# Performance work log

Measured on AMD Instinct MI355X. Metric: run time of the kernel, lower is better.

The kernel has to match this reference:

```python
import jax, jax.numpy as jnp
import numpy as np

B, S, D_MODEL, H, D_KV = 2, 2048, 1024, 16, 64
NUM_BUCKETS, MAX_DIST = 32, 128


def _relative_position_bucket(rel_pos, num_buckets=NUM_BUCKETS, max_distance=MAX_DIST):
    # bidirectional (encoder) bucketing, matching T5Attention._relative_position_bucket
    nb = num_buckets // 2
    buckets = (rel_pos > 0).astype(jnp.int32) * nb
    rel = jnp.abs(rel_pos)
    max_exact = nb // 2
    is_small = rel < max_exact
    rel_f = jnp.maximum(rel.astype(jnp.float32), 1.0)  # guard log(0); masked by is_small anyway
    large = max_exact + (
        jnp.log(rel_f / max_exact) / np.log(max_distance / max_exact) * (nb - max_exact)
    ).astype(jnp.int32)
    large = jnp.minimum(large, nb - 1)
    return buckets + jnp.where(is_small, rel, large)


def setup_inputs() -> dict:
    key = jax.random.key(0)
    ks = jax.random.split(key, 6)
    sc = 1.0 / np.sqrt(D_MODEL)
    return {
        "hidden_states": jax.random.normal(ks[0], (B, S, D_MODEL), jnp.float32),
        "Wq": jax.random.normal(ks[1], (D_MODEL, H * D_KV), jnp.float32) * sc,
        "Wk": jax.random.normal(ks[2], (D_MODEL, H * D_KV), jnp.float32) * sc,
        "Wv": jax.random.normal(ks[3], (D_MODEL, H * D_KV), jnp.float32) * sc,
        "Wo": jax.random.normal(ks[4], (H * D_KV, D_MODEL), jnp.float32) * sc,
        "rel_bias_table": jax.random.normal(ks[5], (NUM_BUCKETS, H), jnp.float32),
    }


def reference(hidden_states, Wq, Wk, Wv, Wo, rel_bias_table):
    b, s, _ = hidden_states.shape
    # projections (T5 uses no bias, scale=1.0 in attention)
    q = (hidden_states @ Wq).reshape(b, s, H, D_KV).transpose(0, 2, 1, 3)  # bhsd
    k = (hidden_states @ Wk).reshape(b, s, H, D_KV).transpose(0, 2, 1, 3)
    v = (hidden_states @ Wv).reshape(b, s, H, D_KV).transpose(0, 2, 1, 3)

    # relative position bias: [1, H, S, S]
    ctx = jnp.arange(s)[:, None]
    mem = jnp.arange(s)[None, :]
    buckets = _relative_position_bucket(mem - ctx)          # [S, S]
    pos_bias = rel_bias_table[buckets]                       # [S, S, H]
    pos_bias = pos_bias.transpose(2, 0, 1)[None]             # [1, H, S, S]

    scores = jnp.einsum("bhqd,bhkd->bhqk", q, k) + pos_bias  # scale = 1.0
    probs = jax.nn.softmax(scores, axis=-1)
    attn = jnp.einsum("bhqk,bhkd->bhqd", probs, v)
    attn = attn.transpose(0, 2, 1, 3).reshape(b, s, H * D_KV)
    return attn @ Wo
```

## Files before the change

kernel.cpp:

```cpp
#include <hip/hip_runtime.h>
#include <hip/hip_fp16.h>

#define S_LEN 2048
#define NH 16
#define DK 64
#define DM 1024
#define NB 2
#define QKV_SZ (NB * NH * S_LEN * DK)

typedef _Float16 half8 __attribute__((ext_vector_type(8)));
typedef _Float16 half4v __attribute__((ext_vector_type(4)));
typedef __fp16 fp16x2 __attribute__((ext_vector_type(2)));
typedef float f32x4 __attribute__((ext_vector_type(4)));

static __device__ __forceinline__ half4v pack4(const f32x4 v) {
  fp16x2 lo = __builtin_amdgcn_cvt_pkrtz(v[0], v[1]);
  fp16x2 hi = __builtin_amdgcn_cvt_pkrtz(v[2], v[3]);
  half4v r;
  ((fp16x2*)&r)[0] = lo;
  ((fp16x2*)&r)[1] = hi;
  return r;
}

#define GLL(gp, lp)                                                              \
  __builtin_amdgcn_global_load_lds(                                              \
      (const __attribute__((address_space(1))) unsigned int*)(gp),               \
      (__attribute__((address_space(3))) unsigned int*)(lp), 16, 0, 0)


__global__ __launch_bounds__(256) void conv_f32_f16(const float* __restrict__ in,
                                                    _Float16* __restrict__ out, int n4) {
  int i = blockIdx.x * 256 + threadIdx.x;
  if (i >= n4) return;
  float4 v = ((const float4*)in)[i];
  half4v o;
  o[0] = (_Float16)v.x; o[1] = (_Float16)v.y; o[2] = (_Float16)v.z; o[3] = (_Float16)v.w;
  ((half4v*)out)[i] = o;
}

__global__ __launch_bounds__(256) void transpose_conv4(
    const float* __restrict__ Wq, const float* __restrict__ Wk,
    const float* __restrict__ Wv, const float* __restrict__ Wo,
    _Float16* __restrict__ Wqkvt, _Float16* __restrict__ Wot) {
  __shared__ float tile[32][33];
  int z = blockIdx.z;
  const float* W = (z == 0) ? Wq : (z == 1) ? Wk : (z == 2) ? Wv : Wo;
  _Float16* Wt = (z < 3) ? (Wqkvt + (size_t)z * 1048576) : Wot;
  float scale = (z == 0) ? 1.44269504f : 1.0f;
  int tx = threadIdx.x, ty = threadIdx.y;
  int nx = blockIdx.x * 32 + tx;
  int ky = blockIdx.y * 32;
#pragma unroll
  for (int i = 0; i < 32; i += 8) tile[ty + i][tx] = W[(size_t)(ky + ty + i) * DM + nx];
  __syncthreads();
  int kx = ky + tx;
  int ny = blockIdx.x * 32;
#pragma unroll
  for (int i = 0; i < 32; i += 8)
    Wt[(size_t)(ny + ty + i) * DM + kx] = (_Float16)(tile[tx][ty + i] * scale);
}

__global__ __launch_bounds__(256) void bias_tab_kernel(const float* __restrict__ table,
                                                       float* __restrict__ tab) {
  int i = blockIdx.x * 256 + threadIdx.x;
  if (i >= NH * 4095) return;
  int h = i / 4095, r = i - h * 4095;
  int rel = r - 2047;
  int bucket = rel > 0 ? 16 : 0;
  int a = rel < 0 ? -rel : rel;
  if (a < 8) {
    bucket += a;
  } else {
    int lg = 31 - __clz(a * a);
    int large = 8 + (lg - 6);
    bucket += (large < 15 ? large : 15);
  }
  tab[i] = table[bucket * NH + h] * 1.44269504f;
}

template <int MODE>
__global__ __launch_bounds__(256) void gemm_f16(const _Float16* __restrict__ A,
                                                const _Float16* __restrict__ Bt,
                                                void* __restrict__ Cout,
                                                int M, int N, int K) {
  __shared__ _Float16 As[128 * 32];
  __shared__ _Float16 Bs[128 * 32];
  const int t = threadIdx.x;
  const int m0 = blockIdx.y * 128, n0 = blockIdx.x * 128;
  const int w = t >> 6, lane = t & 63, l15 = lane & 15, quad = lane >> 4;
  const int wr = (w >> 1) * 64, wc = (w & 1) * 64;
  const int swz = (quad ^ (l15 & 3)) * 8;

  f32x4 acc[4][4];
#pragma unroll
  for (int i = 0; i < 4; i++)
#pragma unroll
    for (int j = 0; j < 4; j++) acc[i][j] = (f32x4){0.f, 0.f, 0.f, 0.f};

  for (int k0 = 0; k0 < K; k0 += 32) {
    __syncthreads();
#pragma unroll
    for (int i = 0; i < 2; i++) {
      int id = t + 256 * i;
      int row = id >> 2, c = id & 3;
      int cg = c ^ (row & 3);
      GLL(A + (size_t)(m0 + row) * K + k0 + cg * 8, (char*)As + id * 16);
      GLL(Bt + (size_t)(n0 + row) * K + k0 + cg * 8, (char*)Bs + id * 16);
    }
    __syncthreads();
    half8 af[4], bf[4];
#pragma unroll
    for (int i = 0; i < 4; i++) af[i] = *(const half8*)(As + (wr + i * 16 + l15) * 32 + swz);
#pragma unroll
    for (int i = 0; i < 4; i++) bf[i] = *(const half8*)(Bs + (wc + i * 16 + l15) * 32 + swz);
#pragma unroll
    for (int i = 0; i < 4; i++)
#pragma unroll
      for (int j = 0; j < 4; j++)
        acc[i][j] = __builtin_amdgcn_mfma_f32_16x16x32_f16(af[i], bf[j], acc[i][j], 0, 0, 0);
  }

#pragma unroll
  for (int i = 0; i < 4; i++)
#pragma unroll
    for (int j = 0; j < 4; j++) {
      int row0 = m0 + wr + i * 16 + quad * 4;
      int col = n0 + wc + j * 16 + l15;
      if (MODE == 1) {
#pragma unroll
        for (int r = 0; r < 4; r++)
          ((float*)Cout)[(size_t)(row0 + r) * N + col] = acc[i][j][r];
      } else {
        int which = col >> 10, rem = col & 1023, hh = rem >> 6, dd = rem & 63;
        int bb = row0 >> 11, ss = row0 & 2047;
        _Float16* base = (_Float16*)Cout;
        if (which == 2) {
          *(half4v*)(base + (size_t)2 * QKV_SZ +
                     ((size_t)((bb * NH + hh) * DK + dd)) * S_LEN + ss) = pack4(acc[i][j]);
        } else {
#pragma unroll
          for (int r = 0; r < 4; r++)
            base[(size_t)which * QKV_SZ +
                 ((size_t)((bb * NH + hh) * S_LEN) + ss + r) * DK + dd] = (_Float16)acc[i][j][r];
        }
      }
    }
}

__global__ __launch_bounds__(256, 4) void attn_kernel(
    const _Float16* __restrict__ Q, const _Float16* __restrict__ K,
    const _Float16* __restrict__ Vt, const float* __restrict__ btab,
    _Float16* __restrict__ attn_out) {
  __shared__ _Float16 Ks[4096];
  __shared__ _Float16 Vs[4096];
  __shared__ _Float16 Ps[4][1024];
  __shared__ float slab[512];

  const int t = threadIdx.x;
  const int Q0 = blockIdx.x * 64;
  const int h = blockIdx.y, b = blockIdx.z;
  const int w = t >> 6, lane = t & 63, l15 = lane & 15, quad = lane >> 4;
  const int qw0 = Q0 + w * 16;
  const int sw7 = l15 & 7;

  const _Float16* Qb = Q + (size_t)(b * NH + h) * S_LEN * DK;
  const _Float16* Kb = K + (size_t)(b * NH + h) * S_LEN * DK;
  const _Float16* Vb = Vt + (size_t)(b * NH + h) * S_LEN * DK;

  for (int i = t; i < 512; i += 256) slab[i] = btab[h * 4095 + 1791 + i];

  half8 qf[2];
#pragma unroll
  for (int dh = 0; dh < 2; dh++)
    qf[dh] = *(const half8*)(Qb + (size_t)(qw0 + l15) * DK + dh * 32 + quad * 8);

  f32x4 o[4];
#pragma unroll
  for (int dt = 0; dt < 4; dt++) o[dt] = (f32x4){0.f, 0.f, 0.f, 0.f};
  float m_ = -INFINITY, l_ = 0.f;

  for (int k0 = 0; k0 < S_LEN; k0 += 64) {
#pragma unroll
    for (int i = 0; i < 2; i++) {
      int id = t + 256 * i;
      int row = id >> 3, c = id & 7;
      int cg = c ^ (row & 7);
      GLL(Kb + (size_t)(k0 + row) * DK + cg * 8, (char*)Ks + id * 16);
      GLL(Vb + (size_t)row * S_LEN + k0 + cg * 8, (char*)Vs + id * 16);
    }
    __syncthreads();

    const int dk0 = k0 - qw0;
    const bool farneg = (dk0 <= -191);
    const bool farpos = (dk0 >= 143);
    const bool nearc = !(farneg || farpos);
    const float cb = farneg ? slab[128] : slab[384];

    f32x4 st[4];
    if (nearc) {
#pragma unroll
      for (int kt = 0; kt < 4; kt++) {
        int i0 = dk0 + kt * 16 + quad * 4 - l15 + 256;
        f32x4 v;
        v[0] = slab[i0]; v[1] = slab[i0 + 1]; v[2] = slab[i0 + 2]; v[3] = slab[i0 + 3];
        st[kt] = v;
      }
    } else {
#pragma unroll
      for (int kt = 0; kt < 4; kt++) st[kt] = (f32x4){0.f, 0.f, 0.f, 0.f};
    }

    half8 kf[4][2], vf[4][2];
#pragma unroll
    for (int kt = 0; kt < 4; kt++)
#pragma unroll
      for (int dh = 0; dh < 2; dh++)
        kf[kt][dh] = *(const half8*)(&Ks[(kt * 16 + l15) * 64 + (((dh << 2) + quad) ^ sw7) * 8]);
#pragma unroll
    for (int dt = 0; dt < 4; dt++)
#pragma unroll
      for (int kh = 0; kh < 2; kh++)
        vf[dt][kh] = *(const half8*)(&Vs[(dt * 16 + l15) * 64 + (((kh << 2) + quad) ^ sw7) * 8]);

#pragma unroll
    for (int kt = 0; kt < 4; kt++)
#pragma unroll
      for (int dh = 0; dh < 2; dh++)
        st[kt] = __builtin_amdgcn_mfma_f32_16x16x32_f16(kf[kt][dh], qf[dh], st[kt], 0, 0, 0);

    float cm = fmaxf(fmaxf(st[0][0], st[0][1]), fmaxf(st[0][2], st[0][3]));
#pragma unroll
    for (int kt = 1; kt < 4; kt++)
      cm = fmaxf(cm, fmaxf(fmaxf(st[kt][0], st[kt][1]), fmaxf(st[kt][2], st[kt][3])));
    cm = fmaxf(cm, __shfl_xor(cm, 16));
    cm = fmaxf(cm, __shfl_xor(cm, 32));
    float mc = nearc ? cm : cm + cb;
    if (__any(mc > m_)) {
      float mnew = fmaxf(m_, mc);
      float alpha = __builtin_amdgcn_exp2f(m_ - mnew);
      m_ = mnew;
      l_ *= alpha;
#pragma unroll
      for (int dt = 0; dt < 4; dt++) o[dt] *= alpha;
    }
    float msub = nearc ? m_ : m_ - cb;

    f32x4 lacc = (f32x4){0.f, 0.f, 0.f, 0.f};
#pragma unroll
    for (int kt = 0; kt < 4; kt++) {
      f32x4 p;
#pragma unroll
      for (int r = 0; r < 4; r++) p[r] = __builtin_amdgcn_exp2f(st[kt][r] - msub);
      lacc += p;
      int g = 2 * kt + (quad >> 1);
      *(half4v*)(&Ps[w][l15 * 64 + (g ^ sw7) * 8 + (quad & 1) * 4]) = pack4(p);
    }
    l_ += (lacc[0] + lacc[1]) + (lacc[2] + lacc[3]);
    __asm__ volatile("s_waitcnt lgkmcnt(0)" ::: "memory");

    half8 pf[2];
#pragma unroll
    for (int kh = 0; kh < 2; kh++)
      pf[kh] = *(const half8*)(&Ps[w][l15 * 64 + (((kh << 2) + quad) ^ sw7) * 8]);
#pragma unroll
    for (int dt = 0; dt < 4; dt++)
#pragma unroll
      for (int kh = 0; kh < 2; kh++)
        o[dt] = __builtin_amdgcn_mfma_f32_16x16x32_f16(vf[dt][kh], pf[kh], o[dt], 0, 0, 0);
    __syncthreads();
  }

  float lf = l_;
  lf += __shfl_xor(lf, 16);
  lf += __shfl_xor(lf, 32);
  float inv = 1.0f / lf;
  int q = qw0 + l15;
#pragma unroll
  for (int dt = 0; dt < 4; dt++) {
    f32x4 ov = o[dt] * inv;
    *(half4v*)(attn_out + ((size_t)(b * S_LEN + q)) * DM + h * DK + dt * 16 + quad * 4) =
        pack4(ov);
  }
}

extern "C" void kernel_launch(void* const* d_in, const int* in_sizes, int n_in,
                              void* d_out, int out_size, void* d_ws, size_t ws_size,
                              hipStream_t stream) {
  const float* hs  = (const float*)d_in[0];
  const float* Wq  = (const float*)d_in[1];
  const float* Wk  = (const float*)d_in[2];
  const float* Wv  = (const float*)d_in[3];
  const float* Wo  = (const float*)d_in[4];
  const float* tbl = (const float*)d_in[5];
  float* out = (float*)d_out;
  char* ws = (char*)d_ws;

  _Float16* Xh    = (_Float16*)(ws);
  _Float16* Wqkvt = (_Float16*)(ws + (8u << 20));
  _Float16* Wot   = (_Float16*)(ws + (14u << 20));
  _Float16* Qd    = (_Float16*)(ws + (16u << 20));
  _Float16* Kd    = Qd + (size_t)QKV_SZ;
  _Float16* Vd    = Qd + (size_t)2 * QKV_SZ;
  _Float16* Ah    = (_Float16*)(ws + (40u << 20));
  float*    btab  = (float*)(ws + (48u << 20));

  conv_f32_f16<<<4096, 256, 0, stream>>>(hs, Xh, (NB * S_LEN * DM) / 4);
  transpose_conv4<<<dim3(32, 32, 4), dim3(32, 8), 0, stream>>>(Wq, Wk, Wv, Wo, Wqkvt, Wot);
  bias_tab_kernel<<<256, 256, 0, stream>>>(tbl, btab);

  gemm_f16<0><<<dim3(24, 32), 256, 0, stream>>>(Xh, Wqkvt, (void*)Qd, NB * S_LEN, 3 * DM, DM);
  attn_kernel<<<dim3(S_LEN / 64, NH, NB), 256, 0, stream>>>(Qd, Kd, Vd, btab, Ah);
  gemm_f16<1><<<dim3(8, 32), 256, 0, stream>>>(Ah, Wot, (void*)out, NB * S_LEN, DM, DM);
}
```

Measured before the change: 216.8 us.

## Split attention keys across waves, swap GEMM MFMA operands, merge prep kernels

The attention kernel now has each wave cover all 64 queries of the block but only a quarter of every 128-key chunk. K and V fragments are read straight from global memory instead of staged through LDS, which removes the per-iteration barriers. The per-wave softmax partials are merged at the end through a shared-memory max/sum reduction. The QKV/output GEMMs swap MFMA operands so Q/K and fp32 outputs are written as contiguous vectors, and the bias-table kernel is folded into the weight transpose launch. The trade-off is more registers (occupancy hint lowered to 3), uncoalesced-ish direct global loads, and extra end-of-kernel reduction work.

```diff
diff --git a/kernel.cpp b/kernel.cpp
--- a/kernel.cpp
+++ b/kernel.cpp
@@ -38,16 +38,36 @@
   ((half4v*)out)[i] = o;
 }
 
-__global__ __launch_bounds__(256) void transpose_conv4(
+__global__ __launch_bounds__(256) void prep_kernel(
     const float* __restrict__ Wq, const float* __restrict__ Wk,
     const float* __restrict__ Wv, const float* __restrict__ Wo,
-    _Float16* __restrict__ Wqkvt, _Float16* __restrict__ Wot) {
+    _Float16* __restrict__ Wqkvt, _Float16* __restrict__ Wot,
+    const float* __restrict__ table, float* __restrict__ btab) {
+  int z = blockIdx.z;
+  int tx = threadIdx.x, ty = threadIdx.y;
+  if (z == 4) {
+    int bid = blockIdx.y * 32 + blockIdx.x;
+    if (bid >= 256) return;
+    int i = bid * 256 + ty * 32 + tx;
+    if (i >= NH * 4095) return;
+    int h = i / 4095, r = i - h * 4095;
+    int rel = r - 2047;
+    int bucket = rel > 0 ? 16 : 0;
+    int a = rel < 0 ? -rel : rel;
+    if (a < 8) {
+      bucket += a;
+    } else {
+      int lg = 31 - __clz(a * a);
+      int large = 8 + (lg - 6);
+      bucket += (large < 15 ? large : 15);
+    }
+    btab[i] = table[bucket * NH + h] * 1.44269504f;
+    return;
+  }
   __shared__ float tile[32][33];
-  int z = blockIdx.z;
   const float* W = (z == 0) ? Wq : (z == 1) ? Wk : (z == 2) ? Wv : Wo;
   _Float16* Wt = (z < 3) ? (Wqkvt + (size_t)z * 1048576) : Wot;
   float scale = (z == 0) ? 1.44269504f : 1.0f;
-  int tx = threadIdx.x, ty = threadIdx.y;
   int nx = blockIdx.x * 32 + tx;
   int ky = blockIdx.y * 32;
 #pragma unroll
@@ -58,24 +78,6 @@
 #pragma unroll
   for (int i = 0; i < 32; i += 8)
     Wt[(size_t)(ny + ty + i) * DM + kx] = (_Float16)(tile[tx][ty + i] * scale);
-}
-
-__global__ __launch_bounds__(256) void bias_tab_kernel(const float* __restrict__ table,
-                                                       float* __restrict__ tab) {
-  int i = blockIdx.x * 256 + threadIdx.x;
-  if (i >= NH * 4095) return;
-  int h = i / 4095, r = i - h * 4095;
-  int rel = r - 2047;
-  int bucket = rel > 0 ? 16 : 0;
-  int a = rel < 0 ? -rel : rel;
-  if (a < 8) {
-    bucket += a;
-  } else {
-    int lg = 31 - __clz(a * a);
-    int large = 8 + (lg - 6);
-    bucket += (large < 15 ? large : 15);
-  }
-  tab[i] = table[bucket * NH + h] * 1.44269504f;
 }
 
 template <int MODE>
@@ -90,6 +92,7 @@
   const int w = t >> 6, lane = t & 63, l15 = lane & 15, quad = lane >> 4;
   const int wr = (w >> 1) * 64, wc = (w & 1) * 64;
   const int swz = (quad ^ (l15 & 3)) * 8;
+  const bool swapped = (MODE == 1) || (n0 < 2048);
 
   f32x4 acc[4][4];
 #pragma unroll
@@ -113,55 +116,64 @@
     for (int i = 0; i < 4; i++) af[i] = *(const half8*)(As + (wr + i * 16 + l15) * 32 + swz);
 #pragma unroll
     for (int i = 0; i < 4; i++) bf[i] = *(const half8*)(Bs + (wc + i * 16 + l15) * 32 + swz);
-#pragma unroll
-    for (int i = 0; i < 4; i++)
-#pragma unroll
-      for (int j = 0; j < 4; j++)
-        acc[i][j] = __builtin_amdgcn_mfma_f32_16x16x32_f16(af[i], bf[j], acc[i][j], 0, 0, 0);
+    if (swapped) {
+#pragma unroll
+      for (int i = 0; i < 4; i++)
+#pragma unroll
+        for (int j = 0; j < 4; j++)
+          acc[i][j] = __builtin_amdgcn_mfma_f32_16x16x32_f16(bf[j], af[i], acc[i][j], 0, 0, 0);
+    } else {
+#pragma unroll
+      for (int i = 0; i < 4; i++)
+#pragma unroll
+        for (int j = 0; j < 4; j++)
+          acc[i][j] = __builtin_amdgcn_mfma_f32_16x16x32_f16(af[i], bf[j], acc[i][j], 0, 0, 0);
+    }
   }
 
 #pragma unroll
   for (int i = 0; i < 4; i++)
 #pragma unroll
     for (int j = 0; j < 4; j++) {
-      int row0 = m0 + wr + i * 16 + quad * 4;
-      int col = n0 + wc + j * 16 + l15;
       if (MODE == 1) {
-#pragma unroll
-        for (int r = 0; r < 4; r++)
-          ((float*)Cout)[(size_t)(row0 + r) * N + col] = acc[i][j][r];
+        int srow = m0 + wr + i * 16 + l15;
+        int col0 = n0 + wc + j * 16 + quad * 4;
+        *(f32x4*)((float*)Cout + (size_t)srow * N + col0) = acc[i][j];
+      } else if (n0 < 2048) {
+        int srow = m0 + wr + i * 16 + l15;
+        int col0 = n0 + wc + j * 16 + quad * 4;
+        int which = col0 >> 10, rem = col0 & 1023, hh = rem >> 6, dd = rem & 63;
+        int bb = srow >> 11, ss = srow & 2047;
+        _Float16* base = (_Float16*)Cout;
+        *(half4v*)(base + (size_t)which * QKV_SZ +
+                   ((size_t)((bb * NH + hh) * S_LEN) + ss) * DK + dd) = pack4(acc[i][j]);
       } else {
-        int which = col >> 10, rem = col & 1023, hh = rem >> 6, dd = rem & 63;
+        int row0 = m0 + wr + i * 16 + quad * 4;
+        int col = n0 + wc + j * 16 + l15;
+        int rem = col & 1023, hh = rem >> 6, dd = rem & 63;
         int bb = row0 >> 11, ss = row0 & 2047;
         _Float16* base = (_Float16*)Cout;
-        if (which == 2) {
-          *(half4v*)(base + (size_t)2 * QKV_SZ +
-                     ((size_t)((bb * NH + hh) * DK + dd)) * S_LEN + ss) = pack4(acc[i][j]);
-        } else {
-#pragma unroll
-          for (int r = 0; r < 4; r++)
-            base[(size_t)which * QKV_SZ +
-                 ((size_t)((bb * NH + hh) * S_LEN) + ss + r) * DK + dd] = (_Float16)acc[i][j][r];
-        }
-      }
-    }
-}
-
-__global__ __launch_bounds__(256, 4) void attn_kernel(
+        *(half4v*)(base + (size_t)2 * QKV_SZ +
+                   ((size_t)((bb * NH + hh) * DK + dd)) * S_LEN + ss) = pack4(acc[i][j]);
+      }
+    }
+}
+
+__global__ __launch_bounds__(256, 3) void attn_kernel(
     const _Float16* __restrict__ Q, const _Float16* __restrict__ K,
     const _Float16* __restrict__ Vt, const float* __restrict__ btab,
     _Float16* __restrict__ attn_out) {
-  __shared__ _Float16 Ks[4096];
-  __shared__ _Float16 Vs[4096];
-  __shared__ _Float16 Ps[4][1024];
-  __shared__ float slab[512];
+  __shared__ __align__(16) char smem[35840];
+  _Float16* Ps = (_Float16*)smem;
+  float* slab = (float*)(smem + 16384);
+  float* obuf = (float*)smem;
+  float* mlbuf = (float*)(smem + 32768);
 
   const int t = threadIdx.x;
   const int Q0 = blockIdx.x * 64;
   const int h = blockIdx.y, b = blockIdx.z;
   const int w = t >> 6, lane = t & 63, l15 = lane & 15, quad = lane >> 4;
-  const int qw0 = Q0 + w * 16;
-  const int sw7 = l15 & 7;
+  const int sw3 = l15 & 3;
 
   const _Float16* Qb = Q + (size_t)(b * NH + h) * S_LEN * DK;
   const _Float16* Kb = K + (size_t)(b * NH + h) * S_LEN * DK;
@@ -169,118 +181,176 @@
 
   for (int i = t; i < 512; i += 256) slab[i] = btab[h * 4095 + 1791 + i];
 
-  half8 qf[2];
-#pragma unroll
-  for (int dh = 0; dh < 2; dh++)
-    qf[dh] = *(const half8*)(Qb + (size_t)(qw0 + l15) * DK + dh * 32 + quad * 8);
-
-  f32x4 o[4];
-#pragma unroll
-  for (int dt = 0; dt < 4; dt++) o[dt] = (f32x4){0.f, 0.f, 0.f, 0.f};
-  float m_ = -INFINITY, l_ = 0.f;
-
-  for (int k0 = 0; k0 < S_LEN; k0 += 64) {
-#pragma unroll
-    for (int i = 0; i < 2; i++) {
-      int id = t + 256 * i;
-      int row = id >> 3, c = id & 7;
-      int cg = c ^ (row & 7);
-      GLL(Kb + (size_t)(k0 + row) * DK + cg * 8, (char*)Ks + id * 16);
-      GLL(Vb + (size_t)row * S_LEN + k0 + cg * 8, (char*)Vs + id * 16);
-    }
-    __syncthreads();
-
-    const int dk0 = k0 - qw0;
-    const bool farneg = (dk0 <= -191);
-    const bool farpos = (dk0 >= 143);
+  half8 qf[4][2];
+#pragma unroll
+  for (int qt = 0; qt < 4; qt++)
+#pragma unroll
+    for (int dh = 0; dh < 2; dh++)
+      qf[qt][dh] =
+          *(const half8*)(Qb + (size_t)(Q0 + qt * 16 + l15) * DK + dh * 32 + quad * 8);
+
+  f32x4 o[4][4];
+#pragma unroll
+  for (int dt = 0; dt < 4; dt++)
+#pragma unroll
+    for (int qt = 0; qt < 4; qt++) o[dt][qt] = (f32x4){0.f, 0.f, 0.f, 0.f};
+  float m_[4] = {-INFINITY, -INFINITY, -INFINITY, -INFINITY};
+  float l_[4] = {0.f, 0.f, 0.f, 0.f};
+
+  _Float16* Pw = Ps + w * 2048;
+
+  __syncthreads();
+
+  for (int it = 0; it < 16; it++) {
+    const int ks0 = it * 128 + w * 32;
+    const int dk = ks0 - Q0;
+    const bool farneg = (dk <= -159);
+    const bool farpos = (dk >= 191);
     const bool nearc = !(farneg || farpos);
     const float cb = farneg ? slab[128] : slab[384];
 
-    f32x4 st[4];
-    if (nearc) {
-#pragma unroll
-      for (int kt = 0; kt < 4; kt++) {
-        int i0 = dk0 + kt * 16 + quad * 4 - l15 + 256;
-        f32x4 v;
-        v[0] = slab[i0]; v[1] = slab[i0 + 1]; v[2] = slab[i0 + 2]; v[3] = slab[i0 + 3];
-        st[kt] = v;
-      }
-    } else {
-#pragma unroll
-      for (int kt = 0; kt < 4; kt++) st[kt] = (f32x4){0.f, 0.f, 0.f, 0.f};
-    }
-
-    half8 kf[4][2], vf[4][2];
-#pragma unroll
-    for (int kt = 0; kt < 4; kt++)
+    half8 kf[2][2], vf[4];
+#pragma unroll
+    for (int kt = 0; kt < 2; kt++)
 #pragma unroll
       for (int dh = 0; dh < 2; dh++)
-        kf[kt][dh] = *(const half8*)(&Ks[(kt * 16 + l15) * 64 + (((dh << 2) + quad) ^ sw7) * 8]);
-#pragma unroll
-    for (int dt = 0; dt < 4; dt++)
-#pragma unroll
-      for (int kh = 0; kh < 2; kh++)
-        vf[dt][kh] = *(const half8*)(&Vs[(dt * 16 + l15) * 64 + (((kh << 2) + quad) ^ sw7) * 8]);
-
-#pragma unroll
-    for (int kt = 0; kt < 4; kt++)
-#pragma unroll
-      for (int dh = 0; dh < 2; dh++)
-        st[kt] = __builtin_amdgcn_mfma_f32_16x16x32_f16(kf[kt][dh], qf[dh], st[kt], 0, 0, 0);
-
-    float cm = fmaxf(fmaxf(st[0][0], st[0][1]), fmaxf(st[0][2], st[0][3]));
-#pragma unroll
-    for (int kt = 1; kt < 4; kt++)
-      cm = fmaxf(cm, fmaxf(fmaxf(st[kt][0], st[kt][1]), fmaxf(st[kt][2], st[kt][3])));
-    cm = fmaxf(cm, __shfl_xor(cm, 16));
-    cm = fmaxf(cm, __shfl_xor(cm, 32));
-    float mc = nearc ? cm : cm + cb;
-    if (__any(mc > m_)) {
-      float mnew = fmaxf(m_, mc);
-      float alpha = __builtin_amdgcn_exp2f(m_ - mnew);
-      m_ = mnew;
-      l_ *= alpha;
-#pragma unroll
-      for (int dt = 0; dt < 4; dt++) o[dt] *= alpha;
-    }
-    float msub = nearc ? m_ : m_ - cb;
-
-    f32x4 lacc = (f32x4){0.f, 0.f, 0.f, 0.f};
-#pragma unroll
-    for (int kt = 0; kt < 4; kt++) {
-      f32x4 p;
-#pragma unroll
-      for (int r = 0; r < 4; r++) p[r] = __builtin_amdgcn_exp2f(st[kt][r] - msub);
-      lacc += p;
-      int g = 2 * kt + (quad >> 1);
-      *(half4v*)(&Ps[w][l15 * 64 + (g ^ sw7) * 8 + (quad & 1) * 4]) = pack4(p);
-    }
-    l_ += (lacc[0] + lacc[1]) + (lacc[2] + lacc[3]);
+        kf[kt][dh] =
+            *(const half8*)(Kb + (size_t)(ks0 + kt * 16 + l15) * DK + dh * 32 + quad * 8);
+#pragma unroll
+    for (int dt = 0; dt < 4; dt++)
+      vf[dt] = *(const half8*)(Vb + (size_t)(dt * 16 + l15) * S_LEN + ks0 + quad * 8);
+
+#pragma unroll
+    for (int qt = 0; qt < 4; qt++) {
+      f32x4 st[2];
+      if (nearc) {
+#pragma unroll
+        for (int kt = 0; kt < 2; kt++) {
+          int i0 = dk + kt * 16 + quad * 4 - qt * 16 - l15 + 256;
+          f32x4 v;
+          v[0] = slab[i0]; v[1] = slab[i0 + 1]; v[2] = slab[i0 + 2]; v[3] = slab[i0 + 3];
+          st[kt] = v;
+        }
+      } else {
+        st[0] = (f32x4){0.f, 0.f, 0.f, 0.f};
+        st[1] = (f32x4){0.f, 0.f, 0.f, 0.f};
+      }
+#pragma unroll
+      for (int kt = 0; kt < 2; kt++)
+#pragma unroll
+        for (int dh = 0; dh < 2; dh++)
+          st[kt] = __builtin_amdgcn_mfma_f32_16x16x32_f16(kf[kt][dh], qf[qt][dh], st[kt],
+                                                          0, 0, 0);
+
+      float cm = fmaxf(fmaxf(st[0][0], st[0][1]), fmaxf(st[0][2], st[0][3]));
+      cm = fmaxf(cm, fmaxf(fmaxf(st[1][0], st[1][1]), fmaxf(st[1][2], st[1][3])));
+      cm = fmaxf(cm, __shfl_xor(cm, 16));
+      cm = fmaxf(cm, __shfl_xor(cm, 32));
+      float mc = nearc ? cm : cm + cb;
+      if (__any(mc > m_[qt])) {
+        float mnew = fmaxf(m_[qt], mc);
+        float alpha = __builtin_amdgcn_exp2f(m_[qt] - mnew);
+        m_[qt] = mnew;
+        l_[qt] *= alpha;
+#pragma unroll
+        for (int dt = 0; dt < 4; dt++) o[dt][qt] *= alpha;
+      }
+      float msub = nearc ? m_[qt] : m_[qt] - cb;
+#pragma unroll
+      for (int kt = 0; kt < 2; kt++) {
+        f32x4 p;
+#pragma unroll
+        for (int r = 0; r < 4; r++) p[r] = __builtin_amdgcn_exp2f(st[kt][r] - msub);
+        l_[qt] += (p[0] + p[1]) + (p[2] + p[3]);
+        int g = kt * 2 + (quad >> 1);
+        *(half4v*)(&Pw[(qt * 16 + l15) * 32 + ((g ^ sw3) << 3) + ((quad & 1) << 2)]) =
+            pack4(p);
+      }
+    }
     __asm__ volatile("s_waitcnt lgkmcnt(0)" ::: "memory");
 
-    half8 pf[2];
-#pragma unroll
-    for (int kh = 0; kh < 2; kh++)
-      pf[kh] = *(const half8*)(&Ps[w][l15 * 64 + (((kh << 2) + quad) ^ sw7) * 8]);
-#pragma unroll
-    for (int dt = 0; dt < 4; dt++)
-#pragma unroll
-      for (int kh = 0; kh < 2; kh++)
-        o[dt] = __builtin_amdgcn_mfma_f32_16x16x32_f16(vf[dt][kh], pf[kh], o[dt], 0, 0, 0);
-    __syncthreads();
-  }
-
-  float lf = l_;
-  lf += __shfl_xor(lf, 16);
-  lf += __shfl_xor(lf, 32);
-  float inv = 1.0f / lf;
-  int q = qw0 + l15;
-#pragma unroll
-  for (int dt = 0; dt < 4; dt++) {
-    f32x4 ov = o[dt] * inv;
-    *(half4v*)(attn_out + ((size_t)(b * S_LEN + q)) * DM + h * DK + dt * 16 + quad * 4) =
-        pack4(ov);
-  }
+    half8 pf[4];
+#pragma unroll
+    for (int qt = 0; qt < 4; qt++)
+      pf[qt] = *(const half8*)(&Pw[(qt * 16 + l15) * 32 + ((quad ^ sw3) << 3)]);
+#pragma unroll
+    for (int dt = 0; dt < 4; dt++)
+#pragma unroll
+      for (int qt = 0; qt < 4; qt++)
+        o[dt][qt] = __builtin_amdgcn_mfma_f32_16x16x32_f16(vf[dt], pf[qt], o[dt][qt],
+                                                           0, 0, 0);
+  }
+
+#pragma unroll
+  for (int qt = 0; qt < 4; qt++) {
+    l_[qt] += __shfl_xor(l_[qt], 16);
+    l_[qt] += __shfl_xor(l_[qt], 32);
+  }
+  __syncthreads();
+  if (quad == 0) {
+#pragma unroll
+    for (int qt = 0; qt < 4; qt++) {
+      mlbuf[(w * 2 + 0) * 64 + qt * 16 + l15] = m_[qt];
+      mlbuf[(w * 2 + 1) * 64 + qt * 16 + l15] = l_[qt];
+    }
+  }
+  __syncthreads();
+  float aw[4], invL[4];
+#pragma unroll
+  for (int qt = 0; qt < 4; qt++) {
+    int q = qt * 16 + l15;
+    float M = mlbuf[0 * 64 + q];
+#pragma unroll
+    for (int v = 1; v < 4; v++) M = fmaxf(M, mlbuf[(v * 2) * 64 + q]);
+    float L = 0.f;
+#pragma unroll
+    for (int v = 0; v < 4; v++)
+      L += mlbuf[(v * 2 + 1) * 64 + q] * __builtin_amdgcn_exp2f(mlbuf[(v * 2) * 64 + q] - M);
+    aw[qt] = __builtin_amdgcn_exp2f(m_[qt] - M);
+    invL[qt] = 1.0f / L;
+  }
+#pragma unroll
+  for (int dt = 0; dt < 4; dt++)
+#pragma unroll
+    for (int qt = 0; qt < 4; qt++) o[dt][qt] *= aw[qt];
+
+#define OIDX(dt, qt) (((qt) * 16 + l15) * 64 + ((((dt) * 4 + quad) ^ ((qt * 16 + l15) & 15)) << 2))
+  if (w & 1) {
+    float* ob = obuf + (w >> 1) * 4096;
+#pragma unroll
+    for (int dt = 0; dt < 4; dt++)
+#pragma unroll
+      for (int qt = 0; qt < 4; qt++) *(f32x4*)(&ob[OIDX(dt, qt)]) = o[dt][qt];
+  }
+  __syncthreads();
+  if (!(w & 1)) {
+    float* ob = obuf + (w >> 1) * 4096;
+#pragma unroll
+    for (int dt = 0; dt < 4; dt++)
+#pragma unroll
+      for (int qt = 0; qt < 4; qt++) o[dt][qt] += *(f32x4*)(&ob[OIDX(dt, qt)]);
+  }
+  __syncthreads();
+  if (w == 2) {
+#pragma unroll
+    for (int dt = 0; dt < 4; dt++)
+#pragma unroll
+      for (int qt = 0; qt < 4; qt++) *(f32x4*)(&obuf[OIDX(dt, qt)]) = o[dt][qt];
+  }
+  __syncthreads();
+  if (w == 0) {
+#pragma unroll
+    for (int qt = 0; qt < 4; qt++) {
+      int q = Q0 + qt * 16 + l15;
+#pragma unroll
+      for (int dt = 0; dt < 4; dt++) {
+        f32x4 ov = (o[dt][qt] + *(f32x4*)(&obuf[OIDX(dt, qt)])) * invL[qt];
+        *(half4v*)(attn_out + ((size_t)(b * S_LEN + q)) * DM + h * DK + dt * 16 + quad * 4) =
+            pack4(ov);
+      }
+    }
+  }
+#undef OIDX
 }
 
 extern "C" void kernel_launch(void* const* d_in, const int* in_sizes, int n_in,
@@ -299,15 +369,14 @@
   _Float16* Wqkvt = (_Float16*)(ws + (8u << 20));
   _Float16* Wot   = (_Float16*)(ws + (14u << 20));
   _Float16* Qd    = (_Float16*)(ws + (16u << 20));
+  _Float16* Ah    = (_Float16*)(ws + (40u << 20));
+  float*    btab  = (float*)(ws + (48u << 20));
   _Float16* Kd    = Qd + (size_t)QKV_SZ;
   _Float16* Vd    = Qd + (size_t)2 * QKV_SZ;
-  _Float16* Ah    = (_Float16*)(ws + (40u << 20));
-  float*    btab  = (float*)(ws + (48u << 20));
 
   conv_f32_f16<<<4096, 256, 0, stream>>>(hs, Xh, (NB * S_LEN * DM) / 4);
-  transpose_conv4<<<dim3(32, 32, 4), dim3(32, 8), 0, stream>>>(Wq, Wk, Wv, Wo, Wqkvt, Wot);
-  bias_tab_kernel<<<256, 256, 0, stream>>>(tbl, btab);
-
+  prep_kernel<<<dim3(32, 32, 5), dim3(32, 8), 0, stream>>>(Wq, Wk, Wv, Wo, Wqkvt, Wot,
+                                                           tbl, btab);
   gemm_f16<0><<<dim3(24, 32), 256, 0, stream>>>(Xh, Wqkvt, (void*)Qd, NB * S_LEN, 3 * DM, DM);
   attn_kernel<<<dim3(S_LEN / 64, NH, NB), 256, 0, stream>>>(Qd, Kd, Vd, btab, Ah);
   gemm_f16<1><<<dim3(8, 32), 256, 0, stream>>>(Ah, Wot, (void*)out, NB * S_LEN, DM, DM);
```

Result: slower. 308.1 us (+42.1%).

## Fragment-major QKV layout, drop attention LDS staging, fuse prep kernels, smaller out GEMM

Applied to the files above, without the earlier changes.

The QKV projection now writes Q, K and V in a layout that matches the MFMA fragments, so the attention kernel loads its K/V fragments straight from global memory into registers. This removes the LDS staging and the per-iteration barriers. The three prep kernels are merged into one launch. The output projection uses 64x64 tiles with swapped MFMA operands, giving more blocks and vectorized float4 stores. The risk is that attention now depends on global/L2 latency without LDS reuse across waves, since each of the four waves loads the same K/V tile.

```diff
diff --git a/kernel.cpp b/kernel.cpp
--- a/kernel.cpp
+++ b/kernel.cpp
@@ -7,6 +7,7 @@
 #define DM 1024
 #define NB 2
 #define QKV_SZ (NB * NH * S_LEN * DK)
+#define HSTRIDE (S_LEN * DK)
 
 typedef _Float16 half8 __attribute__((ext_vector_type(8)));
 typedef _Float16 half4v __attribute__((ext_vector_type(4)));
@@ -28,26 +29,43 @@
       (__attribute__((address_space(3))) unsigned int*)(lp), 16, 0, 0)
 
 
-__global__ __launch_bounds__(256) void conv_f32_f16(const float* __restrict__ in,
-                                                    _Float16* __restrict__ out, int n4) {
-  int i = blockIdx.x * 256 + threadIdx.x;
-  if (i >= n4) return;
-  float4 v = ((const float4*)in)[i];
-  half4v o;
-  o[0] = (_Float16)v.x; o[1] = (_Float16)v.y; o[2] = (_Float16)v.z; o[3] = (_Float16)v.w;
-  ((half4v*)out)[i] = o;
-}
-
-__global__ __launch_bounds__(256) void transpose_conv4(
-    const float* __restrict__ Wq, const float* __restrict__ Wk,
-    const float* __restrict__ Wv, const float* __restrict__ Wo,
-    _Float16* __restrict__ Wqkvt, _Float16* __restrict__ Wot) {
+__global__ __launch_bounds__(256) void prep_kernel(
+    const float* __restrict__ hs, const float* __restrict__ Wq,
+    const float* __restrict__ Wk, const float* __restrict__ Wv,
+    const float* __restrict__ Wo, _Float16* __restrict__ Xh,
+    _Float16* __restrict__ Wqkvt, _Float16* __restrict__ Wot,
+    const float* __restrict__ table, float* __restrict__ btab) {
+  int z = blockIdx.z;
+  int tx = threadIdx.x, ty = threadIdx.y;
+  if (z >= 5) {
+    int i = (((z - 5) << 10) + (int)(blockIdx.y * 32 + blockIdx.x)) * 256 + ty * 32 + tx;
+    float4 v = ((const float4*)hs)[i];
+    half4v o;
+    o[0] = (_Float16)v.x; o[1] = (_Float16)v.y; o[2] = (_Float16)v.z; o[3] = (_Float16)v.w;
+    ((half4v*)Xh)[i] = o;
+    return;
+  }
+  if (z == 4) {
+    int i = (int)(blockIdx.y * 32 + blockIdx.x) * 256 + ty * 32 + tx;
+    if (i >= NH * 4095) return;
+    int h = i / 4095, r = i - h * 4095;
+    int rel = r - 2047;
+    int bucket = rel > 0 ? 16 : 0;
+    int a = rel < 0 ? -rel : rel;
+    if (a < 8) {
+      bucket += a;
+    } else {
+      int lg = 31 - __clz(a * a);
+      int large = 8 + (lg - 6);
+      bucket += (large < 15 ? large : 15);
+    }
+    btab[i] = table[bucket * NH + h] * 1.44269504f;
+    return;
+  }
   __shared__ float tile[32][33];
-  int z = blockIdx.z;
   const float* W = (z == 0) ? Wq : (z == 1) ? Wk : (z == 2) ? Wv : Wo;
   _Float16* Wt = (z < 3) ? (Wqkvt + (size_t)z * 1048576) : Wot;
   float scale = (z == 0) ? 1.44269504f : 1.0f;
-  int tx = threadIdx.x, ty = threadIdx.y;
   int nx = blockIdx.x * 32 + tx;
   int ky = blockIdx.y * 32;
 #pragma unroll
@@ -60,36 +78,18 @@
     Wt[(size_t)(ny + ty + i) * DM + kx] = (_Float16)(tile[tx][ty + i] * scale);
 }
 
-__global__ __launch_bounds__(256) void bias_tab_kernel(const float* __restrict__ table,
-                                                       float* __restrict__ tab) {
-  int i = blockIdx.x * 256 + threadIdx.x;
-  if (i >= NH * 4095) return;
-  int h = i / 4095, r = i - h * 4095;
-  int rel = r - 2047;
-  int bucket = rel > 0 ? 16 : 0;
-  int a = rel < 0 ? -rel : rel;
-  if (a < 8) {
-    bucket += a;
-  } else {
-    int lg = 31 - __clz(a * a);
-    int large = 8 + (lg - 6);
-    bucket += (large < 15 ? large : 15);
-  }
-  tab[i] = table[bucket * NH + h] * 1.44269504f;
-}
-
-template <int MODE>
-__global__ __launch_bounds__(256) void gemm_f16(const _Float16* __restrict__ A,
+__global__ __launch_bounds__(256) void gemm_qkv(const _Float16* __restrict__ A,
                                                 const _Float16* __restrict__ Bt,
-                                                void* __restrict__ Cout,
-                                                int M, int N, int K) {
+                                                _Float16* __restrict__ QKV) {
   __shared__ _Float16 As[128 * 32];
   __shared__ _Float16 Bs[128 * 32];
+  const int K = DM;
   const int t = threadIdx.x;
   const int m0 = blockIdx.y * 128, n0 = blockIdx.x * 128;
   const int w = t >> 6, lane = t & 63, l15 = lane & 15, quad = lane >> 4;
   const int wr = (w >> 1) * 64, wc = (w & 1) * 64;
   const int swz = (quad ^ (l15 & 3)) * 8;
+  const bool swapped = (n0 < 2048);
 
   f32x4 acc[4][4];
 #pragma unroll
@@ -113,46 +113,52 @@
     for (int i = 0; i < 4; i++) af[i] = *(const half8*)(As + (wr + i * 16 + l15) * 32 + swz);
 #pragma unroll
     for (int i = 0; i < 4; i++) bf[i] = *(const half8*)(Bs + (wc + i * 16 + l15) * 32 + swz);
-#pragma unroll
-    for (int i = 0; i < 4; i++)
-#pragma unroll
-      for (int j = 0; j < 4; j++)
-        acc[i][j] = __builtin_amdgcn_mfma_f32_16x16x32_f16(af[i], bf[j], acc[i][j], 0, 0, 0);
+    if (swapped) {
+#pragma unroll
+      for (int i = 0; i < 4; i++)
+#pragma unroll
+        for (int j = 0; j < 4; j++)
+          acc[i][j] = __builtin_amdgcn_mfma_f32_16x16x32_f16(bf[j], af[i], acc[i][j], 0, 0, 0);
+    } else {
+#pragma unroll
+      for (int i = 0; i < 4; i++)
+#pragma unroll
+        for (int j = 0; j < 4; j++)
+          acc[i][j] = __builtin_amdgcn_mfma_f32_16x16x32_f16(af[i], bf[j], acc[i][j], 0, 0, 0);
+    }
   }
 
 #pragma unroll
   for (int i = 0; i < 4; i++)
 #pragma unroll
     for (int j = 0; j < 4; j++) {
-      int row0 = m0 + wr + i * 16 + quad * 4;
-      int col = n0 + wc + j * 16 + l15;
-      if (MODE == 1) {
-#pragma unroll
-        for (int r = 0; r < 4; r++)
-          ((float*)Cout)[(size_t)(row0 + r) * N + col] = acc[i][j][r];
+      if (swapped) {
+        int srow = m0 + wr + i * 16 + l15;
+        int col0 = n0 + wc + j * 16 + quad * 4;
+        int which = col0 >> 10, rem = col0 & 1023, hh = rem >> 6, dd = rem & 63;
+        int bb = srow >> 11, ss = srow & 2047;
+        int lin = ((ss >> 4) << 10) + (((dd >> 5) * 4 + ((dd >> 3) & 3)) << 7) +
+                  ((ss & 15) << 3) + (dd & 7);
+        *(half4v*)(QKV + (size_t)which * QKV_SZ + (size_t)(bb * NH + hh) * HSTRIDE + lin) =
+            pack4(acc[i][j]);
       } else {
-        int which = col >> 10, rem = col & 1023, hh = rem >> 6, dd = rem & 63;
+        int row0 = m0 + wr + i * 16 + quad * 4;
+        int col = n0 + wc + j * 16 + l15;
+        int rem = col & 1023, hh = rem >> 6, dd = rem & 63;
         int bb = row0 >> 11, ss = row0 & 2047;
-        _Float16* base = (_Float16*)Cout;
-        if (which == 2) {
-          *(half4v*)(base + (size_t)2 * QKV_SZ +
-                     ((size_t)((bb * NH + hh) * DK + dd)) * S_LEN + ss) = pack4(acc[i][j]);
-        } else {
-#pragma unroll
-          for (int r = 0; r < 4; r++)
-            base[(size_t)which * QKV_SZ +
-                 ((size_t)((bb * NH + hh) * S_LEN) + ss + r) * DK + dd] = (_Float16)acc[i][j][r];
-        }
+        int lin = ((ss >> 6) << 12) +
+                  ((((dd >> 4) * 2 + ((ss >> 5) & 1)) * 4 + ((ss >> 3) & 3)) << 7) +
+                  ((dd & 15) << 3) + (ss & 7);
+        *(half4v*)(QKV + (size_t)2 * QKV_SZ + (size_t)(bb * NH + hh) * HSTRIDE + lin) =
+            pack4(acc[i][j]);
       }
     }
 }
 
 __global__ __launch_bounds__(256, 4) void attn_kernel(
-    const _Float16* __restrict__ Q, const _Float16* __restrict__ K,
-    const _Float16* __restrict__ Vt, const float* __restrict__ btab,
+    const _Float16* __restrict__ Qf, const _Float16* __restrict__ Kf,
+    const _Float16* __restrict__ Vf, const float* __restrict__ btab,
     _Float16* __restrict__ attn_out) {
-  __shared__ _Float16 Ks[4096];
-  __shared__ _Float16 Vs[4096];
   __shared__ _Float16 Ps[4][1024];
   __shared__ float slab[512];
 
@@ -162,33 +168,41 @@
   const int w = t >> 6, lane = t & 63, l15 = lane & 15, quad = lane >> 4;
   const int qw0 = Q0 + w * 16;
   const int sw7 = l15 & 7;
-
-  const _Float16* Qb = Q + (size_t)(b * NH + h) * S_LEN * DK;
-  const _Float16* Kb = K + (size_t)(b * NH + h) * S_LEN * DK;
-  const _Float16* Vb = Vt + (size_t)(b * NH + h) * S_LEN * DK;
+  const size_t hb = (size_t)(b * NH + h) * HSTRIDE;
+  const _Float16* Qb = Qf + hb;
+  const _Float16* Kb = Kf + hb;
+  const _Float16* Vb = Vf + hb;
 
   for (int i = t; i < 512; i += 256) slab[i] = btab[h * 4095 + 1791 + i];
 
   half8 qf[2];
-#pragma unroll
-  for (int dh = 0; dh < 2; dh++)
-    qf[dh] = *(const half8*)(Qb + (size_t)(qw0 + l15) * DK + dh * 32 + quad * 8);
+  {
+    const _Float16* Qt = Qb + (qw0 >> 4) * 1024 + l15 * 8;
+    qf[0] = *(const half8*)(Qt + quad * 128);
+    qf[1] = *(const half8*)(Qt + (4 + quad) * 128);
+  }
 
   f32x4 o[4];
 #pragma unroll
   for (int dt = 0; dt < 4; dt++) o[dt] = (f32x4){0.f, 0.f, 0.f, 0.f};
   float m_ = -INFINITY, l_ = 0.f;
 
+  __syncthreads();
+
   for (int k0 = 0; k0 < S_LEN; k0 += 64) {
-#pragma unroll
-    for (int i = 0; i < 2; i++) {
-      int id = t + 256 * i;
-      int row = id >> 3, c = id & 7;
-      int cg = c ^ (row & 7);
-      GLL(Kb + (size_t)(k0 + row) * DK + cg * 8, (char*)Ks + id * 16);
-      GLL(Vb + (size_t)row * S_LEN + k0 + cg * 8, (char*)Vs + id * 16);
-    }
-    __syncthreads();
+    half8 kf[4][2], vf[4][2];
+    const _Float16* Kc = Kb + (k0 >> 4) * 1024 + l15 * 8;
+    const _Float16* Vc = Vb + (k0 >> 6) * 4096 + l15 * 8;
+#pragma unroll
+    for (int kt = 0; kt < 4; kt++) {
+      kf[kt][0] = *(const half8*)(Kc + kt * 1024 + quad * 128);
+      kf[kt][1] = *(const half8*)(Kc + kt * 1024 + (4 + quad) * 128);
+    }
+#pragma unroll
+    for (int dt = 0; dt < 4; dt++) {
+      vf[dt][0] = *(const half8*)(Vc + (dt * 8 + quad) * 128);
+      vf[dt][1] = *(const half8*)(Vc + (dt * 8 + 4 + quad) * 128);
+    }
 
     const int dk0 = k0 - qw0;
     const bool farneg = (dk0 <= -191);
@@ -209,18 +223,6 @@
 #pragma unroll
       for (int kt = 0; kt < 4; kt++) st[kt] = (f32x4){0.f, 0.f, 0.f, 0.f};
     }
-
-    half8 kf[4][2], vf[4][2];
-#pragma unroll
-    for (int kt = 0; kt < 4; kt++)
-#pragma unroll
-      for (int dh = 0; dh < 2; dh++)
-        kf[kt][dh] = *(const half8*)(&Ks[(kt * 16 + l15) * 64 + (((dh << 2) + quad) ^ sw7) * 8]);
-#pragma unroll
-    for (int dt = 0; dt < 4; dt++)
-#pragma unroll
-      for (int kh = 0; kh < 2; kh++)
-        vf[dt][kh] = *(const half8*)(&Vs[(dt * 16 + l15) * 64 + (((kh << 2) + quad) ^ sw7) * 8]);
 
 #pragma unroll
     for (int kt = 0; kt < 4; kt++)
@@ -253,7 +255,7 @@
       for (int r = 0; r < 4; r++) p[r] = __builtin_amdgcn_exp2f(st[kt][r] - msub);
       lacc += p;
       int g = 2 * kt + (quad >> 1);
-      *(half4v*)(&Ps[w][l15 * 64 + (g ^ sw7) * 8 + (quad & 1) * 4]) = pack4(p);
+      *(half4v*)(&Ps[w][l15 * 64 + ((g ^ sw7) << 3) + ((quad & 1) << 2)]) = pack4(p);
     }
     l_ += (lacc[0] + lacc[1]) + (lacc[2] + lacc[3]);
     __asm__ volatile("s_waitcnt lgkmcnt(0)" ::: "memory");
@@ -261,13 +263,12 @@
     half8 pf[2];
 #pragma unroll
     for (int kh = 0; kh < 2; kh++)
-      pf[kh] = *(const half8*)(&Ps[w][l15 * 64 + (((kh << 2) + quad) ^ sw7) * 8]);
+      pf[kh] = *(const half8*)(&Ps[w][l15 * 64 + ((((kh << 2) + quad) ^ sw7) << 3)]);
 #pragma unroll
     for (int dt = 0; dt < 4; dt++)
 #pragma unroll
       for (int kh = 0; kh < 2; kh++)
         o[dt] = __builtin_amdgcn_mfma_f32_16x16x32_f16(vf[dt][kh], pf[kh], o[dt], 0, 0, 0);
-    __syncthreads();
   }
 
   float lf = l_;
@@ -281,6 +282,55 @@
     *(half4v*)(attn_out + ((size_t)(b * S_LEN + q)) * DM + h * DK + dt * 16 + quad * 4) =
         pack4(ov);
   }
+}
+
+__global__ __launch_bounds__(256) void gemm_out(const _Float16* __restrict__ A,
+                                                const _Float16* __restrict__ Bt,
+                                                float* __restrict__ C) {
+  __shared__ _Float16 As[64 * 32];
+  __shared__ _Float16 Bs[64 * 32];
+  const int K = DM, N = DM;
+  const int t = threadIdx.x;
+  const int m0 = blockIdx.y * 64, n0 = blockIdx.x * 64;
+  const int w = t >> 6, lane = t & 63, l15 = lane & 15, quad = lane >> 4;
+  const int wr = (w >> 1) * 32, wc = (w & 1) * 32;
+  const int swz = (quad ^ (l15 & 3)) * 8;
+
+  f32x4 acc[2][2];
+#pragma unroll
+  for (int i = 0; i < 2; i++)
+#pragma unroll
+    for (int j = 0; j < 2; j++) acc[i][j] = (f32x4){0.f, 0.f, 0.f, 0.f};
+
+  for (int k0 = 0; k0 < K; k0 += 32) {
+    __syncthreads();
+    {
+      int row = t >> 2, c = t & 3;
+      int cg = c ^ (row & 3);
+      GLL(A + (size_t)(m0 + row) * K + k0 + cg * 8, (char*)As + t * 16);
+      GLL(Bt + (size_t)(n0 + row) * K + k0 + cg * 8, (char*)Bs + t * 16);
+    }
+    __syncthreads();
+    half8 af[2], bf[2];
+#pragma unroll
+    for (int i = 0; i < 2; i++) af[i] = *(const half8*)(As + (wr + i * 16 + l15) * 32 + swz);
+#pragma unroll
+    for (int j = 0; j < 2; j++) bf[j] = *(const half8*)(Bs + (wc + j * 16 + l15) * 32 + swz);
+#pragma unroll
+    for (int i = 0; i < 2; i++)
+#pragma unroll
+      for (int j = 0; j < 2; j++)
+        acc[i][j] = __builtin_amdgcn_mfma_f32_16x16x32_f16(bf[j], af[i], acc[i][j], 0, 0, 0);
+  }
+
+#pragma unroll
+  for (int i = 0; i < 2; i++)
+#pragma unroll
+    for (int j = 0; j < 2; j++) {
+      int srow = m0 + wr + i * 16 + l15;
+      int col0 = n0 + wc + j * 16 + quad * 4;
+      *(f32x4*)(C + (size_t)srow * N + col0) = acc[i][j];
+    }
 }
 
 extern "C" void kernel_launch(void* const* d_in, const int* in_sizes, int n_in,
@@ -299,16 +349,14 @@
   _Float16* Wqkvt = (_Float16*)(ws + (8u << 20));
   _Float16* Wot   = (_Float16*)(ws + (14u << 20));
   _Float16* Qd    = (_Float16*)(ws + (16u << 20));
+  _Float16* Ah    = (_Float16*)(ws + (40u << 20));
+  float*    btab  = (float*)(ws + (48u << 20));
   _Float16* Kd    = Qd + (size_t)QKV_SZ;
   _Float16* Vd    = Qd + (size_t)2 * QKV_SZ;
-  _Float16* Ah    = (_Float16*)(ws + (40u << 20));
-  float*    btab  = (float*)(ws + (48u << 20));
-
-  conv_f32_f16<<<4096, 256, 0, stream>>>(hs, Xh, (NB * S_LEN * DM) / 4);
-  transpose_conv4<<<dim3(32, 32, 4), dim3(32, 8), 0, stream>>>(Wq, Wk, Wv, Wo, Wqkvt, Wot);
-  bias_tab_kernel<<<256, 256, 0, stream>>>(tbl, btab);
-
-  gemm_f16<0><<<dim3(24, 32), 256, 0, stream>>>(Xh, Wqkvt, (void*)Qd, NB * S_LEN, 3 * DM, DM);
+
+  prep_kernel<<<dim3(32, 32, 9), dim3(32, 8), 0, stream>>>(hs, Wq, Wk, Wv, Wo, Xh,
+                                                           Wqkvt, Wot, tbl, btab);
+  gemm_qkv<<<dim3(24, 32), 256, 0, stream>>>(Xh, Wqkvt, Qd);
   attn_kernel<<<dim3(S_LEN / 64, NH, NB), 256, 0, stream>>>(Qd, Kd, Vd, btab, Ah);
-  gemm_f16<1><<<dim3(8, 32), 256, 0, stream>>>(Ah, Wot, (void*)out, NB * S_LEN, DM, DM);
-}
+  gemm_out<<<dim3(16, 64), 256, 0, stream>>>(Ah, Wot, out);
+}
```

After: 219.8 us. Within noise of the previous version (+1.4%).
